# Performance work log

Measured on AMD Instinct MI355X. Metric: run time of the kernel, lower is better.

## Reference

```python
import jax, jax.numpy as jnp
import numpy as np

B, S, D, H, E, TOPK = 4, 2048, 1024, 4096, 8, 2
EPS = 1e-5


def _layernorm(h, g, b):
    mu = jnp.mean(h, axis=-1, keepdims=True)
    var = jnp.mean(jnp.square(h - mu), axis=-1, keepdims=True)
    return (h - mu) * jax.lax.rsqrt(var + EPS) * g + b


def setup_inputs() -> dict:
    key = jax.random.key(0)
    ks = jax.random.split(key, 16)
    s = 0.02
    return {
        "x": jax.random.normal(ks[0], (B, S, D), jnp.float32),
        "context": jax.random.normal(ks[1], (B, S, D), jnp.float32),
        "quality": jax.random.uniform(ks[2], (B,), jnp.float32),
        "rn_g": jnp.ones((D,), jnp.float32), "rn_b": jnp.zeros((D,), jnp.float32),
        "cn_g": jnp.ones((D,), jnp.float32), "cn_b": jnp.zeros((D,), jnp.float32),
        "ctx_W": jax.random.normal(ks[3], (D, D), jnp.float32) * s,
        "ctx_b": jnp.zeros((D,), jnp.float32),
        "q_W": jax.random.normal(ks[4], (1, D), jnp.float32) * s,
        "q_b": jnp.zeros((D,), jnp.float32),
        "r_W": jax.random.normal(ks[5], (D, E), jnp.float32) * s,
        "r_b": jnp.zeros((E,), jnp.float32),
        "temperature": jnp.array(1.0, jnp.float32),
        "W1": jax.random.normal(ks[6], (E, D, H), jnp.float32) * s,
        "b1": jnp.zeros((E, H), jnp.float32),
        "W2": jax.random.normal(ks[7], (E, H, D), jnp.float32) * s,
        "b2": jnp.zeros((E, D), jnp.float32),
    }


def reference(x, context, quality, rn_g, rn_b, cn_g, cn_b, ctx_W, ctx_b,
              q_W, q_b, r_W, r_b, temperature, W1, b1, W2, b2):
    # --- router features (eval mode: no noise, no dropout) ---
    rf = _layernorm(x, rn_g, rn_b)
    rf = rf + _layernorm(context, cn_g, cn_b) @ ctx_W + ctx_b
    # quality [B] -> [B,1,1] -> Linear(1,D) -> [B,1,D], broadcast over seq
    rf = rf + quality[:, None, None] * q_W[0][None, None, :] + q_b

    temp = jnp.maximum(temperature, 0.25)
    logits = (rf @ r_W + r_b) / temp                       # [B,S,E]

    topk_logits, topk_idx = jax.lax.top_k(logits, TOPK)    # [B,S,K]
    gates = jax.nn.softmax(topk_logits, axis=-1)           # [B,S,K]
    # per-expert combine weight: sum_k gate_k * 1[idx_k == e]  -> [B,S,E]
    combine = jnp.sum(jax.nn.one_hot(topk_idx, E, dtype=gates.dtype)
                      * gates[..., None], axis=-2)

    out = jnp.zeros_like(x)
    for e in range(E):  # small fixed expert loop; GEMMs dominate
        h = jax.nn.gelu(x @ W1[e] + b1[e], approximate=False)
        y = h @ W2[e] + b2[e]
        out = out + combine[..., e:e + 1] * y

    # --- aux losses ---
    probs = jax.nn.softmax(logits, axis=-1)
    importance = jnp.mean(probs, axis=(0, 1))              # [E]
    load_balance = jnp.mean(jnp.square(importance - 1.0 / E))
    router_z = jnp.mean(jnp.square(jax.nn.logsumexp(logits, axis=-1)))
    entropy = jnp.mean(-jnp.sum(probs * jnp.log(jnp.clip(probs, 1e-9)), axis=-1))
    aux_total = load_balance + 0.001 * router_z - 0.001 * entropy
    return out, load_balance, router_z, entropy, aux_total
```

## Files before the change

kernel.cpp:

```cpp
#include <hip/hip_runtime.h>
#include <math.h>


typedef unsigned short u16;
typedef __attribute__((ext_vector_type(8))) short short8_t;
typedef __attribute__((ext_vector_type(4))) float f32x4;

#define TOKENS 8192
#define DDIM 1024
#define HDIM 4096
#define NEXP 8
#define ECAP 8192
#define MAX_SLOTS 136
#define NBINS 64

struct __align__(8) us4 { u16 x, y, z, w; };

__device__ __forceinline__ u16 f2bf(float f) {
  unsigned int u = __float_as_uint(f);
  u += 0x7fffu + ((u >> 16) & 1u);
  return (u16)(u >> 16);
}

__device__ __forceinline__ void gload_lds16(const void* g, void* l) {
  __builtin_amdgcn_global_load_lds((const __attribute__((address_space(1))) void*)g,
                                   (__attribute__((address_space(3))) void*)l, 16, 0, 0);
}

__global__ void cvt_bf16_kernel(const float* __restrict__ src, u16* __restrict__ dst, long n) {
  long i = ((long)blockIdx.x * 256 + threadIdx.x) * 4;
  if (i < n) {
    float4 v = *(const float4*)&src[i];
    us4 o; o.x = f2bf(v.x); o.y = f2bf(v.y); o.z = f2bf(v.z); o.w = f2bf(v.w);
    *(us4*)&dst[i] = o;
  }
}

__global__ void transpose_cvt_kernel(const float* __restrict__ src, u16* __restrict__ dst,
                                     int R, int C) {
  __shared__ float tile[32][33];
  size_t mat = (size_t)R * C;
  const float* s = src + (size_t)blockIdx.z * mat;
  u16* d = dst + (size_t)blockIdx.z * mat;
  int r0 = blockIdx.y * 32, c0 = blockIdx.x * 32;
  int tr = threadIdx.x >> 3, tc = (threadIdx.x & 7) * 4;
  float4 v = *(const float4*)&s[(size_t)(r0 + tr) * C + (c0 + tc)];
  tile[tr][tc + 0] = v.x; tile[tr][tc + 1] = v.y;
  tile[tr][tc + 2] = v.z; tile[tr][tc + 3] = v.w;
  __syncthreads();
  int oc = tr, orr = tc;
  us4 o;
  o.x = f2bf(tile[orr + 0][oc]); o.y = f2bf(tile[orr + 1][oc]);
  o.z = f2bf(tile[orr + 2][oc]); o.w = f2bf(tile[orr + 3][oc]);
  *(us4*)&d[(size_t)(c0 + oc) * R + (r0 + orr)] = o;
}

__global__ void crw_kernel(const float* __restrict__ ctxW, const float* __restrict__ rW,
                           float* __restrict__ crW) {
  __shared__ float lbuf[32];
  int d = blockIdx.x, tid = threadIdx.x;
  float acc[8] = {0,0,0,0,0,0,0,0};
  for (int k = tid; k < DDIM; k += 256) {
    float c = ctxW[(size_t)d * DDIM + k];
    float4 r0 = *(const float4*)&rW[k * 8];
    float4 r1 = *(const float4*)&rW[k * 8 + 4];
    acc[0] += c * r0.x; acc[1] += c * r0.y; acc[2] += c * r0.z; acc[3] += c * r0.w;
    acc[4] += c * r1.x; acc[5] += c * r1.y; acc[6] += c * r1.z; acc[7] += c * r1.w;
  }
  int w = tid >> 6, lane = tid & 63;
  #pragma unroll
  for (int off = 32; off; off >>= 1) {
    #pragma unroll
    for (int e = 0; e < 8; e++) acc[e] += __shfl_down(acc[e], off);
  }
  if (lane == 0) {
    #pragma unroll
    for (int e = 0; e < 8; e++) lbuf[w * 8 + e] = acc[e];
  }
  __syncthreads();
  if (tid == 0) {
    #pragma unroll
    for (int e = 0; e < 8; e++)
      crW[d * 8 + e] = lbuf[e] + lbuf[8 + e] + lbuf[16 + e] + lbuf[24 + e];
  }
}

__global__ void cbase_kernel(const float* __restrict__ ctx_b, const float* __restrict__ qW,
                             const float* __restrict__ q_b, const float* __restrict__ quality,
                             const float* __restrict__ rW, const float* __restrict__ r_b,
                             float* __restrict__ cbase) {
  __shared__ float lbuf[32];
  int b = blockIdx.x, tid = threadIdx.x;
  float qv = quality[b];
  float acc[8] = {0,0,0,0,0,0,0,0};
  for (int d = tid; d < DDIM; d += 256) {
    float base = ctx_b[d] + qv * qW[d] + q_b[d];
    float4 r0 = *(const float4*)&rW[d * 8];
    float4 r1 = *(const float4*)&rW[d * 8 + 4];
    acc[0] += base * r0.x; acc[1] += base * r0.y; acc[2] += base * r0.z; acc[3] += base * r0.w;
    acc[4] += base * r1.x; acc[5] += base * r1.y; acc[6] += base * r1.z; acc[7] += base * r1.w;
  }
  int w = tid >> 6, lane = tid & 63;
  #pragma unroll
  for (int off = 32; off; off >>= 1) {
    #pragma unroll
    for (int e = 0; e < 8; e++) acc[e] += __shfl_down(acc[e], off);
  }
  if (lane == 0) {
    #pragma unroll
    for (int e = 0; e < 8; e++) lbuf[w * 8 + e] = acc[e];
  }
  __syncthreads();
  if (tid == 0) {
    #pragma unroll
    for (int e = 0; e < 8; e++)
      cbase[b * 8 + e] = lbuf[e] + lbuf[8 + e] + lbuf[16 + e] + lbuf[24 + e] + r_b[e];
  }
}

__global__ void router_kernel(const float* __restrict__ x, const float* __restrict__ ctx,
    const float* __restrict__ rn_g, const float* __restrict__ rn_b,
    const float* __restrict__ cn_g, const float* __restrict__ cn_b,
    const float* __restrict__ rW, const float* __restrict__ crW,
    const float* __restrict__ cbase, const float* __restrict__ temp_p,
    int* __restrict__ token_list, float* __restrict__ gate_list,
    int* __restrict__ counts, float* __restrict__ aux) {
  __shared__ float rbuf[16];
  __shared__ float lbuf[32];
  const int t = blockIdx.x;
  const int tid = threadIdx.x;
  const int b = t >> 11;
  const float* xr = x + (size_t)t * DDIM;
  const float* cr = ctx + (size_t)t * DDIM;
  float xv[4], cv[4];
  #pragma unroll
  for (int k = 0; k < 4; k++) { int d = tid + k * 256; xv[k] = xr[d]; cv[k] = cr[d]; }
  float sx = 0, sxx = 0, sc = 0, scc = 0;
  #pragma unroll
  for (int k = 0; k < 4; k++) {
    sx += xv[k]; sxx += xv[k] * xv[k];
    sc += cv[k]; scc += cv[k] * cv[k];
  }
  #pragma unroll
  for (int off = 32; off; off >>= 1) {
    sx += __shfl_down(sx, off); sxx += __shfl_down(sxx, off);
    sc += __shfl_down(sc, off); scc += __shfl_down(scc, off);
  }
  int w = tid >> 6, lane = tid & 63;
  if (lane == 0) {
    rbuf[w * 4 + 0] = sx; rbuf[w * 4 + 1] = sxx;
    rbuf[w * 4 + 2] = sc; rbuf[w * 4 + 3] = scc;
  }
  __syncthreads();
  sx  = rbuf[0] + rbuf[4] + rbuf[8]  + rbuf[12];
  sxx = rbuf[1] + rbuf[5] + rbuf[9]  + rbuf[13];
  sc  = rbuf[2] + rbuf[6] + rbuf[10] + rbuf[14];
  scc = rbuf[3] + rbuf[7] + rbuf[11] + rbuf[15];
  const float invD = 1.f / 1024.f;
  float mx = sx * invD, vx = sxx * invD - mx * mx;
  float mc = sc * invD, vc = scc * invD - mc * mc;
  float rsx = rsqrtf(vx + 1e-5f), rsc = rsqrtf(vc + 1e-5f);
  float acc[8] = {0,0,0,0,0,0,0,0};
  #pragma unroll
  for (int k = 0; k < 4; k++) {
    int d = tid + k * 256;
    float lx = (xv[k] - mx) * rsx * rn_g[d] + rn_b[d];
    float lc = (cv[k] - mc) * rsc * cn_g[d] + cn_b[d];
    float4 r0 = *(const float4*)&rW[d * 8];
    float4 r1 = *(const float4*)&rW[d * 8 + 4];
    float4 c0 = *(const float4*)&crW[d * 8];
    float4 c1 = *(const float4*)&crW[d * 8 + 4];
    acc[0] += lx * r0.x + lc * c0.x; acc[1] += lx * r0.y + lc * c0.y;
    acc[2] += lx * r0.z + lc * c0.z; acc[3] += lx * r0.w + lc * c0.w;
    acc[4] += lx * r1.x + lc * c1.x; acc[5] += lx * r1.y + lc * c1.y;
    acc[6] += lx * r1.z + lc * c1.z; acc[7] += lx * r1.w + lc * c1.w;
  }
  #pragma unroll
  for (int off = 32; off; off >>= 1) {
    #pragma unroll
    for (int e = 0; e < 8; e++) acc[e] += __shfl_down(acc[e], off);
  }
  if (lane == 0) {
    #pragma unroll
    for (int e = 0; e < 8; e++) lbuf[w * 8 + e] = acc[e];
  }
  __syncthreads();
  if (tid == 0) {
    float inv_t = 1.f / fmaxf(temp_p[0], 0.25f);
    float lg[8];
    #pragma unroll
    for (int e = 0; e < 8; e++)
      lg[e] = (lbuf[e] + lbuf[8 + e] + lbuf[16 + e] + lbuf[24 + e] + cbase[b * 8 + e]) * inv_t;
    int i0 = 0;
    #pragma unroll
    for (int e = 1; e < 8; e++) if (lg[e] > lg[i0]) i0 = e;
    int i1 = -1;
    #pragma unroll
    for (int e = 0; e < 8; e++) if (e != i0 && (i1 < 0 || lg[e] > lg[i1])) i1 = e;
    float e1v = __expf(lg[i1] - lg[i0]);
    float g0 = 1.f / (1.f + e1v), g1 = e1v / (1.f + e1v);
    float m8 = lg[i0];
    float pe[8], se = 0.f;
    #pragma unroll
    for (int e = 0; e < 8; e++) { pe[e] = expf(lg[e] - m8); se += pe[e]; }
    float inv_se = 1.f / se;
    float z = m8 + logf(se);
    float entc = 0.f;
    #pragma unroll
    for (int e = 0; e < 8; e++) {
      float p = pe[e] * inv_se;
      entc -= p * logf(fmaxf(p, 1e-9f));
    }
    int bin = (t & (NBINS - 1)) * 12;
    #pragma unroll
    for (int e = 0; e < 8; e++) atomicAdd(&aux[bin + e], pe[e] * inv_se);
    atomicAdd(&aux[bin + 8], z * z);
    atomicAdd(&aux[bin + 9], entc);
    int p0 = atomicAdd(&counts[i0], 1);
    token_list[i0 * ECAP + p0] = t; gate_list[i0 * ECAP + p0] = g0;
    int p1 = atomicAdd(&counts[i1], 1);
    token_list[i1 * ECAP + p1] = t; gate_list[i1 * ECAP + p1] = g1;
  }
}

__global__ void finalize_kernel(const int* __restrict__ counts, const float* __restrict__ aux,
                                int* __restrict__ token_list, float* __restrict__ gate_list,
                                int4* __restrict__ table, float* __restrict__ out_scalars) {
  __shared__ int scnt[NEXP], stl[NEXP], sbase[NEXP];
  __shared__ float sred[16];
  const int tid = threadIdx.x;
  if (tid < NEXP) {
    int c = counts[tid];
    scnt[tid] = c;
    stl[tid] = (c + 127) >> 7;
  }
  __syncthreads();
  if (tid == 0) {
    int s = 0;
    for (int e = 0; e < NEXP; e++) { sbase[e] = s; s += stl[e]; }
  }
  __syncthreads();
  for (int slot = tid; slot < MAX_SLOTS; slot += 256) {
    int4 v = make_int4(-1, 0, 0, 0);
    #pragma unroll
    for (int e = 0; e < NEXP; e++) {
      int rel = slot - sbase[e];
      if (rel >= 0 && rel < stl[e]) {
        int rv = scnt[e] - rel * 128;
        if (rv > 128) rv = 128;
        v = make_int4(e, rel * 128, rv, 0);
      }
    }
    table[slot] = v;
  }
  for (int idx = tid; idx < NEXP * 128; idx += 256) {
    int e = idx >> 7, p = idx & 127;
    int pos = scnt[e] + p;
    if (pos < stl[e] * 128) {
      token_list[e * ECAP + pos] = 0;
      gate_list[e * ECAP + pos] = 0.f;
    }
  }
  if (tid < 10) {
    float s = 0.f;
    #pragma unroll 8
    for (int bn = 0; bn < NBINS; bn++) s += aux[bn * 12 + tid];
    sred[tid] = s;
  }
  __syncthreads();
  if (tid == 0) {
    float lb = 0.f;
    #pragma unroll
    for (int e = 0; e < NEXP; e++) {
      float im = sred[e] * (1.f / 8192.f);
      float dd = im - 0.125f;
      lb += dd * dd;
    }
    lb *= (1.f / 8.f);
    float rz = sred[8] * (1.f / 8192.f);
    float ent = sred[9] * (1.f / 8192.f);
    out_scalars[0] = lb;
    out_scalars[1] = rz;
    out_scalars[2] = ent;
    out_scalars[3] = lb + 0.001f * rz - 0.001f * ent;
  }
}

template <int MODE>
__launch_bounds__(256, 3)
__global__ void moe_gemm_kernel(const u16* __restrict__ Asrc, const u16* __restrict__ Bt,
    const float* __restrict__ bias, const int* __restrict__ token_list,
    const float* __restrict__ gate_list, const int4* __restrict__ table,
    u16* __restrict__ h_out, float* __restrict__ out) {
  constexpr int KD = (MODE == 0) ? DDIM : HDIM;
  constexpr int ND = (MODE == 0) ? HDIM : DDIM;
  const int slot = blockIdx.y;
  const int4 tb = table[slot];
  const int e = tb.x;
  if (e < 0) return;
  const int row0 = tb.y, rv = tb.z;
  const int n0 = blockIdx.x * 128;
  const int tid = threadIdx.x;
  const int lane = tid & 63, w = tid >> 6;

  __shared__ __align__(16) u16 As[128 * 64];
  __shared__ __align__(16) u16 Bs[128 * 64];

  const u16* aptr[4];
  const u16* bptr[4];
  const u16* bbase = Bt + (size_t)e * ((size_t)ND * KD);
  #pragma unroll
  for (int i = 0; i < 4; i++) {
    int q = i * 256 + tid;
    int row = q >> 3, ch = q & 7;
    size_t abase;
    if (MODE == 0) {
      int tok = token_list[e * ECAP + row0 + row];
      abase = (size_t)tok * KD;
    } else {
      abase = ((size_t)slot * 128 + row) * (size_t)KD;
    }
    aptr[i] = Asrc + abase + ch * 8;
    bptr[i] = bbase + (size_t)(n0 + row) * KD + ch * 8;
  }

  f32x4 acc[4][4];
  #pragma unroll
  for (int i = 0; i < 4; i++) {
    #pragma unroll
    for (int j = 0; j < 4; j++) acc[i][j] = (f32x4){0.f, 0.f, 0.f, 0.f};
  }

  const int lr = lane & 15, quad = lane >> 4;
  const int wm = (w & 1) * 64, wn = (w >> 1) * 64;

  for (int k0 = 0; k0 < KD; k0 += 64) {
    #pragma unroll
    for (int i = 0; i < 4; i++) {
      gload_lds16(aptr[i] + k0, &As[(i * 256 + tid) * 8]);
      gload_lds16(bptr[i] + k0, &Bs[(i * 256 + tid) * 8]);
    }
    __syncthreads();
    #pragma unroll
    for (int kk = 0; kk < 2; kk++) {
      short8_t a[4], b[4];
      #pragma unroll
      for (int i = 0; i < 4; i++)
        a[i] = *(const short8_t*)&As[(wm + i * 16 + lr) * 64 + kk * 32 + quad * 8];
      #pragma unroll
      for (int j = 0; j < 4; j++)
        b[j] = *(const short8_t*)&Bs[(wn + j * 16 + lr) * 64 + kk * 32 + quad * 8];
      #pragma unroll
      for (int i = 0; i < 4; i++) {
        #pragma unroll
        for (int j = 0; j < 4; j++)
          acc[i][j] = __builtin_amdgcn_mfma_f32_16x16x32_bf16(a[i], b[j], acc[i][j], 0, 0, 0);
      }
    }
    __syncthreads();
  }

  float bcol[4];
  #pragma unroll
  for (int j = 0; j < 4; j++) bcol[j] = bias[e * ND + n0 + wn + j * 16 + lr];

  if constexpr (MODE == 0) {
    #pragma unroll
    for (int i = 0; i < 4; i++) {
      #pragma unroll
      for (int r = 0; r < 4; r++) {
        int row = wm + i * 16 + quad * 4 + r;
        size_t ro = ((size_t)slot * 128 + row) * (size_t)HDIM;
        #pragma unroll
        for (int j = 0; j < 4; j++) {
          int col = n0 + wn + j * 16 + lr;
          float v = acc[i][j][r] + bcol[j];
          v = 0.5f * v * (1.f + erff(v * 0.70710678118654752f));
          h_out[ro + col] = f2bf(v);
        }
      }
    }
  } else {
    #pragma unroll
    for (int i = 0; i < 4; i++) {
      #pragma unroll
      for (int r = 0; r < 4; r++) {
        int row = wm + i * 16 + quad * 4 + r;
        if (row < rv) {
          int tok = token_list[e * ECAP + row0 + row];
          float g = gate_list[e * ECAP + row0 + row];
          float* orow = out + (size_t)tok * DDIM;
          #pragma unroll
          for (int j = 0; j < 4; j++) {
            int col = n0 + wn + j * 16 + lr;
            atomicAdd(&orow[col], g * (acc[i][j][r] + bcol[j]));
          }
        }
      }
    }
  }
}

extern "C" void kernel_launch(void* const* d_in, const int* in_sizes, int n_in,
                              void* d_out, int out_size, void* d_ws, size_t ws_size,
                              hipStream_t stream) {
  const float* x      = (const float*)d_in[0];
  const float* ctx    = (const float*)d_in[1];
  const float* qual   = (const float*)d_in[2];
  const float* rn_g   = (const float*)d_in[3];
  const float* rn_b   = (const float*)d_in[4];
  const float* cn_g   = (const float*)d_in[5];
  const float* cn_b   = (const float*)d_in[6];
  const float* ctx_W  = (const float*)d_in[7];
  const float* ctx_b  = (const float*)d_in[8];
  const float* q_W    = (const float*)d_in[9];
  const float* q_b    = (const float*)d_in[10];
  const float* r_W    = (const float*)d_in[11];
  const float* r_b    = (const float*)d_in[12];
  const float* temp   = (const float*)d_in[13];
  const float* W1     = (const float*)d_in[14];
  const float* b1     = (const float*)d_in[15];
  const float* W2     = (const float*)d_in[16];
  const float* b2     = (const float*)d_in[17];
  float* out = (float*)d_out;

  char* ws = (char*)d_ws;
  size_t o = 0;
  auto alloc = [&](size_t bytes) { void* p = ws + o; o += (bytes + 255) & ~(size_t)255; return p; };
  u16*   xbf        = (u16*)alloc((size_t)TOKENS * DDIM * 2);
  u16*   W1t        = (u16*)alloc((size_t)NEXP * HDIM * DDIM * 2);
  u16*   W2t        = (u16*)alloc((size_t)NEXP * DDIM * HDIM * 2);
  u16*   hbuf       = (u16*)alloc((size_t)MAX_SLOTS * 128 * HDIM * 2);
  float* crW        = (float*)alloc(DDIM * 8 * 4);
  float* cb         = (float*)alloc(32 * 4);
  int*   token_list = (int*)alloc(NEXP * ECAP * 4);
  float* gate_list  = (float*)alloc(NEXP * ECAP * 4);
  int*   counts     = (int*)alloc((8 + NBINS * 12) * 4);
  float* aux        = (float*)(counts + 8);
  int4*  table      = (int4*)alloc(MAX_SLOTS * 16);
  (void)ws_size; (void)n_in; (void)in_sizes;

  (void)hipMemsetAsync(d_out, 0, (size_t)out_size * 4, stream);
  (void)hipMemsetAsync(counts, 0, (8 + NBINS * 12) * 4, stream);

  cvt_bf16_kernel<<<(TOKENS * DDIM) / 1024, 256, 0, stream>>>(x, xbf, (long)TOKENS * DDIM);
  transpose_cvt_kernel<<<dim3(HDIM / 32, DDIM / 32, NEXP), 256, 0, stream>>>(W1, W1t, DDIM, HDIM);
  transpose_cvt_kernel<<<dim3(DDIM / 32, HDIM / 32, NEXP), 256, 0, stream>>>(W2, W2t, HDIM, DDIM);
  crw_kernel<<<DDIM, 256, 0, stream>>>(ctx_W, r_W, crW);
  cbase_kernel<<<4, 256, 0, stream>>>(ctx_b, q_W, q_b, qual, r_W, r_b, cb);
  router_kernel<<<TOKENS, 256, 0, stream>>>(x, ctx, rn_g, rn_b, cn_g, cn_b, r_W, crW, cb, temp,
                                            token_list, gate_list, counts, aux);
  finalize_kernel<<<1, 256, 0, stream>>>(counts, aux, token_list, gate_list, table,
                                         out + (size_t)TOKENS * DDIM);
  moe_gemm_kernel<0><<<dim3(HDIM / 128, MAX_SLOTS), 256, 0, stream>>>(
      xbf, W1t, b1, token_list, gate_list, table, hbuf, nullptr);
  moe_gemm_kernel<1><<<dim3(DDIM / 128, MAX_SLOTS), 256, 0, stream>>>(
      hbuf, W2t, b2, token_list, gate_list, table, nullptr, out);
}
```

Baseline: 1.060 ms.

## Enlarge MoE GEMM tiles to 256x256 with 8 waves, double-buffered LDS pipeline

Replaces the 128x128 single-buffered expert GEMM with a 256x256 tile over 512 threads. It stages two k-tiles at once in a 128KB LDS buffer with XOR swizzling and hand-placed barriers and waitcnts, interleaving loads with MFMA groups that run at raised priority. The second GEMM is split in two along K to restore grid parallelism, with bias added only in the first split, and the expert slot granularity moves from 128 to 256 tokens. The aim is better data reuse per loaded byte and overlap of global loads with compute. The cost is more padding waste per expert, lower occupancy from the large LDS footprint, and twice as many atomic adds in the output.

```diff
diff --git a/kernel.cpp b/kernel.cpp
--- a/kernel.cpp
+++ b/kernel.cpp
@@ -11,7 +11,7 @@
 #define HDIM 4096
 #define NEXP 8
 #define ECAP 8192
-#define MAX_SLOTS 136
+#define MAX_SLOTS 71
 #define NBINS 64
 
 struct __align__(8) us4 { u16 x, y, z, w; };
@@ -232,7 +232,7 @@
   if (tid < NEXP) {
     int c = counts[tid];
     scnt[tid] = c;
-    stl[tid] = (c + 127) >> 7;
+    stl[tid] = (c + 255) >> 8;
   }
   __syncthreads();
   if (tid == 0) {
@@ -246,17 +246,17 @@
     for (int e = 0; e < NEXP; e++) {
       int rel = slot - sbase[e];
       if (rel >= 0 && rel < stl[e]) {
-        int rv = scnt[e] - rel * 128;
-        if (rv > 128) rv = 128;
-        v = make_int4(e, rel * 128, rv, 0);
+        int rv = scnt[e] - rel * 256;
+        if (rv > 256) rv = 256;
+        v = make_int4(e, rel * 256, rv, 0);
       }
     }
     table[slot] = v;
   }
-  for (int idx = tid; idx < NEXP * 128; idx += 256) {
-    int e = idx >> 7, p = idx & 127;
+  for (int idx = tid; idx < NEXP * 256; idx += 256) {
+    int e = idx >> 8, p = idx & 255;
     int pos = scnt[e] + p;
-    if (pos < stl[e] * 128) {
+    if (pos < stl[e] * 256) {
       token_list[e * ECAP + pos] = 0;
       gate_list[e * ECAP + pos] = 0.f;
     }
@@ -286,94 +286,156 @@
   }
 }
 
+
+#define BAR   asm volatile("s_barrier" ::: "memory")
+#define LGKM0 asm volatile("s_waitcnt lgkmcnt(0)" ::: "memory")
+#define VMC8  asm volatile("s_waitcnt vmcnt(8)" ::: "memory")
+#define VMC0  asm volatile("s_waitcnt vmcnt(0)" ::: "memory")
+
 template <int MODE>
-__launch_bounds__(256, 3)
-__global__ void moe_gemm_kernel(const u16* __restrict__ Asrc, const u16* __restrict__ Bt,
+__launch_bounds__(512, 2)
+__global__ void moe_gemm8_kernel(const u16* __restrict__ Asrc, const u16* __restrict__ Bt,
     const float* __restrict__ bias, const int* __restrict__ token_list,
     const float* __restrict__ gate_list, const int4* __restrict__ table,
     u16* __restrict__ h_out, float* __restrict__ out) {
-  constexpr int KD = (MODE == 0) ? DDIM : HDIM;
-  constexpr int ND = (MODE == 0) ? HDIM : DDIM;
+  constexpr int KSTRIDE = (MODE == 0) ? DDIM : HDIM;
+  constexpr int ND      = (MODE == 0) ? HDIM : DDIM;
+  constexpr int NT      = (MODE == 0) ? (DDIM / 64) : (2048 / 64);
+  constexpr int ITERS   = NT / 2;
+
   const int slot = blockIdx.y;
   const int4 tb = table[slot];
   const int e = tb.x;
   if (e < 0) return;
   const int row0 = tb.y, rv = tb.z;
-  const int n0 = blockIdx.x * 128;
+  const int n0 = blockIdx.x * 256;
+  const int kz = (MODE == 1) ? blockIdx.z : 0;
+  const int kbase = kz * 2048;
+
   const int tid = threadIdx.x;
   const int lane = tid & 63, w = tid >> 6;
-
-  __shared__ __align__(16) u16 As[128 * 64];
-  __shared__ __align__(16) u16 Bs[128 * 64];
-
-  const u16* aptr[4];
-  const u16* bptr[4];
-  const u16* bbase = Bt + (size_t)e * ((size_t)ND * KD);
-  #pragma unroll
-  for (int i = 0; i < 4; i++) {
-    int q = i * 256 + tid;
-    int row = q >> 3, ch = q & 7;
-    size_t abase;
-    if (MODE == 0) {
-      int tok = token_list[e * ECAP + row0 + row];
-      abase = (size_t)tok * KD;
-    } else {
-      abase = ((size_t)slot * 128 + row) * (size_t)KD;
-    }
-    aptr[i] = Asrc + abase + ch * 8;
-    bptr[i] = bbase + (size_t)(n0 + row) * KD + ch * 8;
-  }
-
-  f32x4 acc[4][4];
-  #pragma unroll
-  for (int i = 0; i < 4; i++) {
+  const int lr = lane & 15, quad = lane >> 4;
+
+  __shared__ __align__(16) u16 lds[65536];
+
+  const u16* bbase = Bt + (size_t)e * ((size_t)ND * KSTRIDE);
+  const u16* pA[2][2];
+  const u16* pB[2][2];
+  #pragma unroll
+  for (int j = 0; j < 2; ++j) {
+    int c = j * 512 + tid;
+    int r = c >> 3;
+    int kc = (c & 7) ^ (r & 7);
+    #pragma unroll
+    for (int h = 0; h < 2; ++h) {
+      if constexpr (MODE == 0) {
+        int tok = token_list[e * ECAP + row0 + h * 128 + r];
+        pA[h][j] = Asrc + (size_t)tok * KSTRIDE + kc * 8;
+      } else {
+        pA[h][j] = Asrc + ((size_t)slot * 256 + h * 128 + r) * (size_t)KSTRIDE + kbase + kc * 8;
+      }
+      pB[h][j] = bbase + (size_t)(n0 + h * 128 + r) * KSTRIDE + kbase + kc * 8;
+    }
+  }
+
+#define STAGE_A(h, tt) do { int _bo = ((tt)&1)*32768 + (h)*8192; \
+    gload_lds16(pA[h][0] + (tt)*64, &lds[_bo + tid*8]); \
+    gload_lds16(pA[h][1] + (tt)*64, &lds[_bo + 4096 + tid*8]); } while (0)
+#define STAGE_B(h, tt) do { int _bo = ((tt)&1)*32768 + 16384 + (h)*8192; \
+    gload_lds16(pB[h][0] + (tt)*64, &lds[_bo + tid*8]); \
+    gload_lds16(pB[h][1] + (tt)*64, &lds[_bo + 4096 + tid*8]); } while (0)
+
+  const int aRow = ((w >> 2) * 128 + lr) * 64;
+  const int bRow = 16384 + ((w & 3) * 64 + lr) * 64;
+  const int kx0 = ((0 + quad) ^ (lr & 7)) * 8;
+  const int kx1 = ((4 + quad) ^ (lr & 7)) * 8;
+
+  f32x4 acc[8][4];
+  #pragma unroll
+  for (int i = 0; i < 8; i++)
     #pragma unroll
     for (int j = 0; j < 4; j++) acc[i][j] = (f32x4){0.f, 0.f, 0.f, 0.f};
-  }
-
-  const int lr = lane & 15, quad = lane >> 4;
-  const int wm = (w & 1) * 64, wn = (w >> 1) * 64;
-
-  for (int k0 = 0; k0 < KD; k0 += 64) {
-    #pragma unroll
-    for (int i = 0; i < 4; i++) {
-      gload_lds16(aptr[i] + k0, &As[(i * 256 + tid) * 8]);
-      gload_lds16(bptr[i] + k0, &Bs[(i * 256 + tid) * 8]);
-    }
-    __syncthreads();
-    #pragma unroll
-    for (int kk = 0; kk < 2; kk++) {
-      short8_t a[4], b[4];
-      #pragma unroll
-      for (int i = 0; i < 4; i++)
-        a[i] = *(const short8_t*)&As[(wm + i * 16 + lr) * 64 + kk * 32 + quad * 8];
-      #pragma unroll
-      for (int j = 0; j < 4; j++)
-        b[j] = *(const short8_t*)&Bs[(wn + j * 16 + lr) * 64 + kk * 32 + quad * 8];
-      #pragma unroll
-      for (int i = 0; i < 4; i++) {
-        #pragma unroll
-        for (int j = 0; j < 4; j++)
-          acc[i][j] = __builtin_amdgcn_mfma_f32_16x16x32_bf16(a[i], b[j], acc[i][j], 0, 0, 0);
-      }
-    }
-    __syncthreads();
-  }
+
+  short8_t a[4][2], b[2][2];
+
+#define LDA(MQ, BUF) do { const u16* _p = &lds[(BUF)*32768 + aRow + (MQ)*4096]; \
+    a[0][0] = *(const short8_t*)(_p + kx0);        a[0][1] = *(const short8_t*)(_p + kx1); \
+    a[1][0] = *(const short8_t*)(_p + 1024 + kx0); a[1][1] = *(const short8_t*)(_p + 1024 + kx1); \
+    a[2][0] = *(const short8_t*)(_p + 2048 + kx0); a[2][1] = *(const short8_t*)(_p + 2048 + kx1); \
+    a[3][0] = *(const short8_t*)(_p + 3072 + kx0); a[3][1] = *(const short8_t*)(_p + 3072 + kx1); \
+  } while (0)
+#define LDB(NQ, BUF) do { const u16* _p = &lds[(BUF)*32768 + bRow + (NQ)*2048]; \
+    b[0][0] = *(const short8_t*)(_p + kx0);        b[0][1] = *(const short8_t*)(_p + kx1); \
+    b[1][0] = *(const short8_t*)(_p + 1024 + kx0); b[1][1] = *(const short8_t*)(_p + 1024 + kx1); \
+  } while (0)
+#define MMA(MQ, NQ) do { \
+    __builtin_amdgcn_s_setprio(1); \
+    _Pragma("unroll") \
+    for (int kk2 = 0; kk2 < 2; ++kk2) \
+      _Pragma("unroll") \
+      for (int i2 = 0; i2 < 4; ++i2) \
+        _Pragma("unroll") \
+        for (int j2 = 0; j2 < 2; ++j2) \
+          acc[(MQ)*4 + i2][(NQ)*2 + j2] = __builtin_amdgcn_mfma_f32_16x16x32_bf16( \
+              a[i2][kk2], b[j2][kk2], acc[(MQ)*4 + i2][(NQ)*2 + j2], 0, 0, 0); \
+    __builtin_amdgcn_s_setprio(0); \
+  } while (0)
+
+  STAGE_A(0, 0); STAGE_A(1, 0); STAGE_B(0, 0); STAGE_B(1, 0);
+  STAGE_A(0, 1); STAGE_A(1, 1); STAGE_B(0, 1); STAGE_B(1, 1);
+  VMC8;
+  BAR;
+
+  for (int it = 0; it < ITERS; ++it) {
+    const int v = 2 * it + 1, u2 = 2 * it + 2;
+    const bool sv = (it > 0), su = (u2 < NT);
+    LDA(0, 0); LDB(0, 0);
+    if (sv) { STAGE_A(0, v); STAGE_A(1, v); }
+    BAR; LGKM0; MMA(0, 0); BAR;
+    LDB(1, 0);
+    if (sv) { STAGE_B(0, v); STAGE_B(1, v); }
+    BAR; LGKM0; MMA(0, 1); BAR;
+    LDA(1, 0);
+    BAR; LGKM0; MMA(1, 1); BAR;
+    LDB(0, 0);
+    VMC0;
+    BAR; LGKM0; MMA(1, 0); BAR;
+    LDA(0, 1); LDB(0, 1);
+    if (su) { STAGE_A(0, u2); STAGE_A(1, u2); }
+    BAR; LGKM0; MMA(0, 0); BAR;
+    LDB(1, 1);
+    if (su) { STAGE_B(0, u2); STAGE_B(1, u2); }
+    BAR; LGKM0; MMA(0, 1); BAR;
+    LDA(1, 1);
+    BAR; LGKM0; MMA(1, 1); BAR;
+    LDB(0, 1);
+    VMC0;
+    BAR; LGKM0; MMA(1, 0); BAR;
+  }
+
+#undef STAGE_A
+#undef STAGE_B
+#undef LDA
+#undef LDB
+#undef MMA
 
   float bcol[4];
   #pragma unroll
-  for (int j = 0; j < 4; j++) bcol[j] = bias[e * ND + n0 + wn + j * 16 + lr];
+  for (int j = 0; j < 4; j++) {
+    int col = n0 + (w & 3) * 64 + j * 16 + lr;
+    bcol[j] = (MODE == 1 && kz != 0) ? 0.f : bias[e * ND + col];
+  }
 
   if constexpr (MODE == 0) {
     #pragma unroll
-    for (int i = 0; i < 4; i++) {
+    for (int i = 0; i < 8; i++) {
       #pragma unroll
       for (int r = 0; r < 4; r++) {
-        int row = wm + i * 16 + quad * 4 + r;
-        size_t ro = ((size_t)slot * 128 + row) * (size_t)HDIM;
+        int row = (w >> 2) * 128 + i * 16 + quad * 4 + r;
+        size_t ro = ((size_t)slot * 256 + row) * (size_t)HDIM;
         #pragma unroll
         for (int j = 0; j < 4; j++) {
-          int col = n0 + wn + j * 16 + lr;
+          int col = n0 + (w & 3) * 64 + j * 16 + lr;
           float v = acc[i][j][r] + bcol[j];
           v = 0.5f * v * (1.f + erff(v * 0.70710678118654752f));
           h_out[ro + col] = f2bf(v);
@@ -382,17 +444,17 @@
     }
   } else {
     #pragma unroll
-    for (int i = 0; i < 4; i++) {
+    for (int i = 0; i < 8; i++) {
       #pragma unroll
       for (int r = 0; r < 4; r++) {
-        int row = wm + i * 16 + quad * 4 + r;
+        int row = (w >> 2) * 128 + i * 16 + quad * 4 + r;
         if (row < rv) {
           int tok = token_list[e * ECAP + row0 + row];
           float g = gate_list[e * ECAP + row0 + row];
           float* orow = out + (size_t)tok * DDIM;
           #pragma unroll
           for (int j = 0; j < 4; j++) {
-            int col = n0 + wn + j * 16 + lr;
+            int col = n0 + (w & 3) * 64 + j * 16 + lr;
             atomicAdd(&orow[col], g * (acc[i][j][r] + bcol[j]));
           }
         }
@@ -430,7 +492,7 @@
   u16*   xbf        = (u16*)alloc((size_t)TOKENS * DDIM * 2);
   u16*   W1t        = (u16*)alloc((size_t)NEXP * HDIM * DDIM * 2);
   u16*   W2t        = (u16*)alloc((size_t)NEXP * DDIM * HDIM * 2);
-  u16*   hbuf       = (u16*)alloc((size_t)MAX_SLOTS * 128 * HDIM * 2);
+  u16*   hbuf       = (u16*)alloc((size_t)MAX_SLOTS * 256 * HDIM * 2);
   float* crW        = (float*)alloc(DDIM * 8 * 4);
   float* cb         = (float*)alloc(32 * 4);
   int*   token_list = (int*)alloc(NEXP * ECAP * 4);
@@ -452,8 +514,8 @@
                                             token_list, gate_list, counts, aux);
   finalize_kernel<<<1, 256, 0, stream>>>(counts, aux, token_list, gate_list, table,
                                          out + (size_t)TOKENS * DDIM);
-  moe_gemm_kernel<0><<<dim3(HDIM / 128, MAX_SLOTS), 256, 0, stream>>>(
+  moe_gemm8_kernel<0><<<dim3(HDIM / 256, MAX_SLOTS), 512, 0, stream>>>(
       xbf, W1t, b1, token_list, gate_list, table, hbuf, nullptr);
-  moe_gemm_kernel<1><<<dim3(DDIM / 128, MAX_SLOTS), 256, 0, stream>>>(
+  moe_gemm8_kernel<1><<<dim3(DDIM / 256, MAX_SLOTS, 2), 512, 0, stream>>>(
       hbuf, W2t, b2, token_list, gate_list, table, nullptr, out);
 }
```

After: 1.173 ms. 1.11x slower.
